# Kernel tuning notes

Measured on AMD Instinct MI355X. Metric: run time of the kernel, lower is better.

The kernel has to match this reference:

```python
import jax, jax.numpy as jnp
import numpy as np

H = 16  # hidden size = time_slot(=32) / 2
G = 3 * H  # gate dim (r|z|n), torch gate order


def _gru_dir(x, Wi, Wh, bi, bh, reverse):
    """Single-direction GRU over time. x: [B,T,F]; Wi:[3H,F]; Wh:[3H,H]."""
    xp = jnp.einsum('btf,gf->btg', x, Wi) + bi  # [B,T,3H] input projections, all steps at once
    if reverse:
        xp = xp[:, ::-1]
    xp_t = jnp.swapaxes(xp, 0, 1)  # [T,B,3H]
    h0 = jnp.zeros((x.shape[0], H), x.dtype)

    def step(h, g_x):
        g_h = h @ Wh.T + bh  # [B,3H]
        r = jax.nn.sigmoid(g_x[:, :H] + g_h[:, :H])
        z = jax.nn.sigmoid(g_x[:, H:2 * H] + g_h[:, H:2 * H])
        n = jnp.tanh(g_x[:, 2 * H:] + r * g_h[:, 2 * H:])
        h_new = (1.0 - z) * n + z * h
        return h_new, h_new

    _, ys = jax.lax.scan(step, h0, xp_t)
    ys = jnp.swapaxes(ys, 0, 1)  # [B,T,H]
    if reverse:
        ys = ys[:, ::-1]
    return ys


def _bigru(x, Wi, Wh, bi, bh):
    """Bidirectional GRU layer; params indexed [dir(2), ...]."""
    fwd = _gru_dir(x, Wi[0], Wh[0], bi[0], bh[0], False)
    bwd = _gru_dir(x, Wi[1], Wh[1], bi[1], bh[1], True)
    return jnp.concatenate([fwd, bwd], axis=-1)  # [B,T,2H]


def setup_inputs() -> dict:
    key = jax.random.key(0)
    ks = jax.random.split(key, 12)
    B, T, F_IN, DEPTH, NCLS = 16384, 64, 3, 5, 4
    s = 0.25  # ~1/sqrt(H) torch init scale
    return {
        'x': jax.random.normal(ks[0], (B, T, F_IN), jnp.float32),
        # GRU1: 1 layer, 2 directions, input 3
        'Wi1': jax.random.normal(ks[1], (2, G, F_IN), jnp.float32) * s,
        'Wh1': jax.random.normal(ks[2], (2, G, H), jnp.float32) * s,
        'bi1': jax.random.normal(ks[3], (2, G), jnp.float32) * s,
        'bh1': jax.random.normal(ks[4], (2, G), jnp.float32) * s,
        # GRU5: 5 layers, 2 directions, input 2H=32 every layer
        'Wi5': jax.random.normal(ks[5], (DEPTH, 2, G, 2 * H), jnp.float32) * s,
        'Wh5': jax.random.normal(ks[6], (DEPTH, 2, G, H), jnp.float32) * s,
        'bi5': jax.random.normal(ks[7], (DEPTH, 2, G), jnp.float32) * s,
        'bh5': jax.random.normal(ks[8], (DEPTH, 2, G), jnp.float32) * s,
        # classifier Linear(2H -> num_class)
        'Wc': jax.random.normal(ks[9], (NCLS, 2 * H), jnp.float32) * s,
        'bc': jax.random.normal(ks[10], (NCLS,), jnp.float32) * s,
    }


def reference(x, Wi1, Wh1, bi1, bh1, Wi5, Wh5, bi5, bh5, Wc, bc):
    y = _bigru(x, Wi1, Wh1, bi1, bh1)  # [B,T,2H]
    for l in range(Wi5.shape[0]):  # 5 stacked bi-GRU layers
        y = _bigru(y, Wi5[l], Wh5[l], bi5[l], bh5[l])
    logits = jnp.einsum('btd,cd->btc', y, Wc) + bc  # [B,T,num_class]
    return jax.nn.softmax(logits, axis=2)
```

## Files before the change

kernel.cpp:

```cpp
#include <hip/hip_runtime.h>

#define T 64
#define F_IN 3
#define H 16
#define G 48
#define D2 32
#define DEPTH 5
#define NCLS 4
#define L2E 1.44269504f

#define YST 32
#define YSB 2048
#define HZ_ZOFF 64

typedef _Float16 half8 __attribute__((ext_vector_type(8)));
typedef float f32x4v __attribute__((ext_vector_type(4)));

__device__ __forceinline__ float fexp2(float x) { return __builtin_amdgcn_exp2f(x); }
__device__ __forceinline__ float frcp(float x)  { return __builtin_amdgcn_rcpf(x); }

__global__ __launch_bounds__(128, 3) void bigru_all(
    const float* __restrict__ x,
    const float* __restrict__ Wi1, const float* __restrict__ Wh1,
    const float* __restrict__ bi1, const float* __restrict__ bh1,
    const float* __restrict__ Wi5, const float* __restrict__ Wh5,
    const float* __restrict__ bi5, const float* __restrict__ bh5,
    const float* __restrict__ Wc,  const float* __restrict__ bc,
    float* __restrict__ out)
{
    __shared__ __align__(16) _Float16 yb[2][2 * YSB];
    __shared__ __align__(16) _Float16 hzb[2][80];
    __shared__ __align__(16) float xls[2][512];

    const int wv   = threadIdx.x >> 6;
    const int lane = threadIdx.x & 63;
    const int pair = blockIdx.x * 2 + wv;

    _Float16* ybw  = yb[wv];
    _Float16* hzbw = hzb[wv];
    float*    xlsw = xls[wv];

    const int j15  = lane & 15;
    const int quad = lane >> 4;
    const int lb   = quad & 1;
    const int dir  = quad >> 1;
    const bool isf = (dir == 0);

    hzbw[lane] = (_Float16)0.0f;
    if (lane < 16) hzbw[64 + lane] = (_Float16)0.0f;

    {
        const float* xg0 = x + (size_t)pair * (2 * T * F_IN);
        #pragma unroll
        for (int k = 0; k < 2; ++k) {
            int idx = lane + 64 * k;
            float a0 = xg0[3 * idx], a1 = xg0[3 * idx + 1], a2 = xg0[3 * idx + 2];
            float4 v; v.x = a0; v.y = a1; v.z = a2; v.w = 0.0f;
            *(float4*)(xlsw + 4 * idx) = v;
        }
    }

    const int  job_a  = j15 >> 2;
    const bool avalid = ((j15 >> 3) == 0) ? (quad < 2) : (quad >= 2);
    const _Float16* aptr = hzbw + (avalid ? (job_a * 16 + (quad & 1) * 8) : HZ_ZOFF);

    const int ystep = isf ? YST : -YST;
    const f32x4v zC = {0.f, 0.f, 0.f, 0.f};
    const int klo = (quad & 1) * 8;
    const int bdir = (quad < 2) ? 0 : 1;

    float hj;
    half8 ag = *(const half8*)aptr;

    {
        half8 whB[3];
        {
            const float* wsrc = Wh1 + bdir * (G * H);
            #pragma unroll
            for (int g = 0; g < 3; ++g) {
                const float scale = (g == 2) ? (-2.0f * L2E) : L2E;
                const float* w = wsrc + (g * 16 + j15) * H + klo;
                half8 hv;
                #pragma unroll
                for (int i = 0; i < 8; ++i) hv[i] = (_Float16)(scale * w[i]);
                whB[g] = hv;
            }
        }
        float wi[3][F_IN];
        float bir[3], bhn2;
        {
            const float* Wi = Wi1 + dir * (G * F_IN);
            const float* bi = bi1 + dir * G;
            const float* bh = bh1 + dir * G;
            #pragma unroll
            for (int g = 0; g < 3; ++g) {
                const float scale = (g == 2) ? (-2.0f * L2E) : L2E;
                int row = g * H + j15;
                #pragma unroll
                for (int k = 0; k < F_IN; ++k) wi[g][k] = scale * Wi[row * F_IN + k];
                bir[g] = scale * bi[row] + ((g < 2) ? (L2E * bh[row]) : 0.0f);
            }
            bhn2 = -2.0f * L2E * bh[2 * H + j15];
        }
        const f32x4v cN = {bhn2, bhn2, bhn2, bhn2};
        hj = 0.0f;

        int xi = lb * 64 + (isf ? 0 : (T - 1));
        const int xstep = isf ? 1 : -1;
        _Float16* yw = ybw + lb * YSB + (isf ? 0 : (T - 1)) * YST + dir * H + j15;

        #pragma unroll 4
        for (int s = 0; s < T; ++s) {
            float4 xv = *(const float4*)(xlsw + 4 * xi);
            xi += xstep;
            float gxr = fmaf(wi[0][2], xv.z, fmaf(wi[0][1], xv.y, fmaf(wi[0][0], xv.x, bir[0])));
            float gxz = fmaf(wi[1][2], xv.z, fmaf(wi[1][1], xv.y, fmaf(wi[1][0], xv.x, bir[1])));
            float gxn = fmaf(wi[2][2], xv.z, fmaf(wi[2][1], xv.y, fmaf(wi[2][0], xv.x, bir[2])));
            f32x4v d0 = __builtin_amdgcn_mfma_f32_16x16x32_f16(ag, whB[0], zC, 0, 0, 0);
            f32x4v d1 = __builtin_amdgcn_mfma_f32_16x16x32_f16(ag, whB[1], zC, 0, 0, 0);
            f32x4v d2 = __builtin_amdgcn_mfma_f32_16x16x32_f16(ag, whB[2], cN, 0, 0, 0);
            float av = gxr + d0[0];
            float bv = gxz + d1[0];
            float Er = fexp2(-av);
            float Ez = fexp2(-bv);
            float rg = frcp(1.0f + Er);
            float c2 = fmaf(rg, d2[0], gxn);
            float Ec = fexp2(c2);
            float dz = 1.0f + Ez;
            float num = fmaf(hj - Ez, Ec, hj + Ez);
            float den = fmaf(dz, Ec, dz);
            float hn = num * frcp(den);
            hj = hn;
            _Float16 hh = (_Float16)hn;
            hzbw[lane] = hh;
            ag = *(const half8*)aptr;
            *yw = hh;
            yw += ystep;
        }
    }

    #pragma unroll 1
    for (int l = 0; l < DEPTH; ++l) {
        half8 bflo[3], bfhi[3];
        #pragma unroll
        for (int g = 0; g < 3; ++g) {
            const float scale = (g == 2) ? (-2.0f * L2E) : L2E;
            const float* w = Wi5 + ((size_t)(l * 2 + bdir) * G + g * 16 + j15) * D2;
            half8 lo, hi;
            #pragma unroll
            for (int i = 0; i < 8; ++i) {
                lo[i] = (_Float16)(scale * w[klo + i]);
                hi[i] = (_Float16)(scale * w[16 + klo + i]);
            }
            bflo[g] = lo;
            bfhi[g] = hi;
        }
        half8 whB[3];
        {
            const float* wsrc = Wh5 + ((size_t)(l * 2) + bdir) * G * H;
            #pragma unroll
            for (int g = 0; g < 3; ++g) {
                const float scale = (g == 2) ? (-2.0f * L2E) : L2E;
                const float* w = wsrc + (g * 16 + j15) * H + klo;
                half8 hv;
                #pragma unroll
                for (int i = 0; i < 8; ++i) hv[i] = (_Float16)(scale * w[i]);
                whB[g] = hv;
            }
        }
        float bib0, bib1, bib2, bhn2;
        {
            const float* biL = bi5 + (l * 2 + dir) * G;
            const float* bhL = bh5 + (l * 2 + dir) * G;
            bib0 = L2E * (biL[j15]     + bhL[j15]);
            bib1 = L2E * (biL[H + j15] + bhL[H + j15]);
            bib2 = -2.0f * L2E * biL[2 * H + j15];
            bhn2 = -2.0f * L2E * bhL[2 * H + j15];
        }
        const f32x4v cR  = {bib0, bib0, bib0, bib0};
        const f32x4v cZ  = {bib1, bib1, bib1, bib1};
        const f32x4v cNx = {bib2, bib2, bib2, bib2};
        const f32x4v cN  = {bhn2, bhn2, bhn2, bhn2};

        hj = 0.0f;
        hzbw[lane] = (_Float16)0.0f;
        ag = *(const half8*)aptr;

        const bool fsel = (j15 < 8);
        const int  lb_a = (j15 >> 2) & 1;
        const int  tl_a = j15 & 3;
        const bool axv  = fsel ? (quad < 2) : (quad >= 2);

        const _Float16* ap;
        int apstep, hioff;
        if (axv) {
            ap     = ybw + lb_a * YSB + (fsel ? tl_a : (T - 1 - tl_a)) * YST + klo;
            apstep = fsel ? (4 * YST) : -(4 * YST);
            hioff  = 16;
        } else {
            ap     = hzbw + HZ_ZOFF;
            apstep = 0;
            hioff  = 0;
        }

        unsigned int ypk[16];

        #pragma unroll
        for (int c = 0; c < 8; ++c) {
            half8 alo = *(const half8*)ap;
            half8 ahi = *(const half8*)(ap + hioff);
            ap += apstep;
            f32x4v c0 = __builtin_amdgcn_mfma_f32_16x16x32_f16(alo, bflo[0], cR, 0, 0, 0);
            f32x4v c1 = __builtin_amdgcn_mfma_f32_16x16x32_f16(alo, bflo[1], cZ, 0, 0, 0);
            f32x4v c2g = __builtin_amdgcn_mfma_f32_16x16x32_f16(alo, bflo[2], cNx, 0, 0, 0);
            c0  = __builtin_amdgcn_mfma_f32_16x16x32_f16(ahi, bfhi[0], c0, 0, 0, 0);
            c1  = __builtin_amdgcn_mfma_f32_16x16x32_f16(ahi, bfhi[1], c1, 0, 0, 0);
            c2g = __builtin_amdgcn_mfma_f32_16x16x32_f16(ahi, bfhi[2], c2g, 0, 0, 0);

            #pragma unroll
            for (int s = 0; s < 4; ++s) {
                f32x4v d0 = __builtin_amdgcn_mfma_f32_16x16x32_f16(ag, whB[0], c0, 0, 0, 0);
                f32x4v d1 = __builtin_amdgcn_mfma_f32_16x16x32_f16(ag, whB[1], c1, 0, 0, 0);
                f32x4v d2 = __builtin_amdgcn_mfma_f32_16x16x32_f16(ag, whB[2], cN, 0, 0, 0);
                float Er = fexp2(-d0[s]);
                float Ez = fexp2(-d1[s]);
                float rg = frcp(1.0f + Er);
                float cc = fmaf(rg, d2[0], c2g[s]);
                float Ec = fexp2(cc);
                float dz = 1.0f + Ez;
                float num = fmaf(hj - Ez, Ec, hj + Ez);
                float den = fmaf(dz, Ec, dz);
                float hn = num * frcp(den);
                hj = hn;
                _Float16 hh = (_Float16)hn;
                hzbw[lane] = hh;
                ag = *(const half8*)aptr;
                unsigned int hb16 = (unsigned int)__builtin_bit_cast(unsigned short, hh);
                if (s & 1) ypk[2 * c + (s >> 1)] |= hb16 << 16;
                else       ypk[2 * c + (s >> 1)]  = hb16;
            }
        }

        {
            _Float16* yw = ybw + lb * YSB + (isf ? 32 : 31) * YST + dir * H + j15;
            #pragma unroll 1
            for (int c = 8; c < 16; ++c) {
                half8 alo = *(const half8*)ap;
                half8 ahi = *(const half8*)(ap + hioff);
                ap += apstep;
                f32x4v c0 = __builtin_amdgcn_mfma_f32_16x16x32_f16(alo, bflo[0], cR, 0, 0, 0);
                f32x4v c1 = __builtin_amdgcn_mfma_f32_16x16x32_f16(alo, bflo[1], cZ, 0, 0, 0);
                f32x4v c2g = __builtin_amdgcn_mfma_f32_16x16x32_f16(alo, bflo[2], cNx, 0, 0, 0);
                c0  = __builtin_amdgcn_mfma_f32_16x16x32_f16(ahi, bfhi[0], c0, 0, 0, 0);
                c1  = __builtin_amdgcn_mfma_f32_16x16x32_f16(ahi, bfhi[1], c1, 0, 0, 0);
                c2g = __builtin_amdgcn_mfma_f32_16x16x32_f16(ahi, bfhi[2], c2g, 0, 0, 0);

                unsigned int w01 = 0, w23 = 0;
                #pragma unroll
                for (int s = 0; s < 4; ++s) {
                    f32x4v d0 = __builtin_amdgcn_mfma_f32_16x16x32_f16(ag, whB[0], c0, 0, 0, 0);
                    f32x4v d1 = __builtin_amdgcn_mfma_f32_16x16x32_f16(ag, whB[1], c1, 0, 0, 0);
                    f32x4v d2 = __builtin_amdgcn_mfma_f32_16x16x32_f16(ag, whB[2], cN, 0, 0, 0);
                    float Er = fexp2(-d0[s]);
                    float Ez = fexp2(-d1[s]);
                    float rg = frcp(1.0f + Er);
                    float cc = fmaf(rg, d2[0], c2g[s]);
                    float Ec = fexp2(cc);
                    float dz = 1.0f + Ez;
                    float num = fmaf(hj - Ez, Ec, hj + Ez);
                    float den = fmaf(dz, Ec, dz);
                    float hn = num * frcp(den);
                    hj = hn;
                    _Float16 hh = (_Float16)hn;
                    hzbw[lane] = hh;
                    ag = *(const half8*)aptr;
                    unsigned int hb16 = (unsigned int)__builtin_bit_cast(unsigned short, hh);
                    if (s & 1) { if (s >> 1) w23 |= hb16 << 16; else w01 |= hb16 << 16; }
                    else       { if (s >> 1) w23  = hb16;       else w01  = hb16; }
                }
                *yw = __builtin_bit_cast(_Float16, (unsigned short)(w01 & 0xffffu)); yw += ystep;
                *yw = __builtin_bit_cast(_Float16, (unsigned short)(w01 >> 16));     yw += ystep;
                *yw = __builtin_bit_cast(_Float16, (unsigned short)(w23 & 0xffffu)); yw += ystep;
                *yw = __builtin_bit_cast(_Float16, (unsigned short)(w23 >> 16));     yw += ystep;
            }
        }

        {
            _Float16* yw = ybw + lb * YSB + (isf ? 0 : (T - 1)) * YST + dir * H + j15;
            #pragma unroll
            for (int i = 0; i < 16; ++i) {
                unsigned int v = ypk[i];
                *yw = __builtin_bit_cast(_Float16, (unsigned short)(v & 0xffffu));
                yw += ystep;
                *yw = __builtin_bit_cast(_Float16, (unsigned short)(v >> 16));
                yw += ystep;
            }
        }
    }

    #pragma unroll
    for (int i = 0; i < 2; ++i) {
        int idx = lane + i * 64;
        int bb  = idx >> 6;
        int t   = idx & 63;
        const _Float16* yrow = ybw + bb * YSB + t * YST;
        float yv[D2];
        #pragma unroll
        for (int k8 = 0; k8 < 4; ++k8) {
            half8 v = *(const half8*)(yrow + k8 * 8);
            #pragma unroll
            for (int i8 = 0; i8 < 8; ++i8) yv[k8 * 8 + i8] = (float)v[i8];
        }
        float lg[NCLS];
        #pragma unroll
        for (int c = 0; c < NCLS; ++c) {
            const float* wc = Wc + c * D2;
            float acc = bc[c];
            #pragma unroll
            for (int k = 0; k < D2; ++k) acc = fmaf(wc[k], yv[k], acc);
            lg[c] = acc;
        }
        float m = fmaxf(fmaxf(lg[0], lg[1]), fmaxf(lg[2], lg[3]));
        float e0 = __expf(lg[0] - m), e1 = __expf(lg[1] - m);
        float e2 = __expf(lg[2] - m), e3 = __expf(lg[3] - m);
        float inv = frcp(e0 + e1 + e2 + e3);
        size_t bglob = (size_t)pair * 2 + bb;
        float4 o;
        o.x = e0 * inv; o.y = e1 * inv; o.z = e2 * inv; o.w = e3 * inv;
        ((float4*)out)[bglob * T + t] = o;
    }
}

extern "C" void kernel_launch(void* const* d_in, const int* in_sizes, int n_in,
                              void* d_out, int out_size, void* d_ws, size_t ws_size,
                              hipStream_t stream) {
    const float* x   = (const float*)d_in[0];
    const float* Wi1 = (const float*)d_in[1];
    const float* Wh1 = (const float*)d_in[2];
    const float* bi1 = (const float*)d_in[3];
    const float* bh1 = (const float*)d_in[4];
    const float* Wi5 = (const float*)d_in[5];
    const float* Wh5 = (const float*)d_in[6];
    const float* bi5 = (const float*)d_in[7];
    const float* bh5 = (const float*)d_in[8];
    const float* Wc  = (const float*)d_in[9];
    const float* bc  = (const float*)d_in[10];
    float* out = (float*)d_out;

    const int B = in_sizes[0] / (T * F_IN);
    dim3 grid(B / 4), block(128);
    hipLaunchKernelGGL(bigru_all, grid, block, 0, stream,
                       x, Wi1, Wh1, bi1, bh1, Wi5, Wh5, bi5, bh5, Wc, bc, out);
}
```

Baseline: 310.3 us.

## Ping-pong LDS sequence buffers and launch one wave per block

Each block now runs a single wavefront on one batch pair. A double-buffered LDS area (P0/P1) alternates source and destination per layer, so each layer writes its hidden states straight to the other buffer. This replaces the old scheme that parked the first half of the outputs in registers (ypk) and split the time loop into two variants. The goal is lower register pressure, simpler code and removal of the inter-wave shared-memory layout. The cost is more LDS per wavefront (about 16 KB versus about 10 KB before), which may limit how many waves fit on a CU.

```diff
diff --git a/kernel.cpp b/kernel.cpp
--- a/kernel.cpp
+++ b/kernel.cpp
@@ -19,7 +19,7 @@
 __device__ __forceinline__ float fexp2(float x) { return __builtin_amdgcn_exp2f(x); }
 __device__ __forceinline__ float frcp(float x)  { return __builtin_amdgcn_rcpf(x); }
 
-__global__ __launch_bounds__(128, 3) void bigru_all(
+__global__ __launch_bounds__(64, 3) void bigru_all(
     const float* __restrict__ x,
     const float* __restrict__ Wi1, const float* __restrict__ Wh1,
     const float* __restrict__ bi1, const float* __restrict__ bh1,
@@ -28,18 +28,13 @@
     const float* __restrict__ Wc,  const float* __restrict__ bc,
     float* __restrict__ out)
 {
-    __shared__ __align__(16) _Float16 yb[2][2 * YSB];
-    __shared__ __align__(16) _Float16 hzb[2][80];
-    __shared__ __align__(16) float xls[2][512];
-
-    const int wv   = threadIdx.x >> 6;
-    const int lane = threadIdx.x & 63;
-    const int pair = blockIdx.x * 2 + wv;
-
-    _Float16* ybw  = yb[wv];
-    _Float16* hzbw = hzb[wv];
-    float*    xlsw = xls[wv];
-
+    __shared__ __align__(16) _Float16 S[4 * YSB + 80];
+    _Float16* const P0   = S;
+    _Float16* const P1   = S + 2 * YSB;
+    _Float16* const hzbw = S + 4 * YSB;
+    float*    const xlsw = (float*)P1;
+
+    const int lane = threadIdx.x;
     const int j15  = lane & 15;
     const int quad = lane >> 4;
     const int lb   = quad & 1;
@@ -50,7 +45,7 @@
     if (lane < 16) hzbw[64 + lane] = (_Float16)0.0f;
 
     {
-        const float* xg0 = x + (size_t)pair * (2 * T * F_IN);
+        const float* xg0 = x + (size_t)blockIdx.x * (2 * T * F_IN);
         #pragma unroll
         for (int k = 0; k < 2; ++k) {
             int idx = lane + 64 * k;
@@ -107,7 +102,7 @@
 
         int xi = lb * 64 + (isf ? 0 : (T - 1));
         const int xstep = isf ? 1 : -1;
-        _Float16* yw = ybw + lb * YSB + (isf ? 0 : (T - 1)) * YST + dir * H + j15;
+        _Float16* yw = P0 + lb * YSB + (isf ? 0 : (T - 1)) * YST + dir * H + j15;
 
         #pragma unroll 4
         for (int s = 0; s < T; ++s) {
@@ -141,6 +136,9 @@
 
     #pragma unroll 1
     for (int l = 0; l < DEPTH; ++l) {
+        _Float16* const ysrc = (l & 1) ? P1 : P0;
+        _Float16* const ydst = (l & 1) ? P0 : P1;
+
         half8 bflo[3], bfhi[3];
         #pragma unroll
         for (int g = 0; g < 3; ++g) {
@@ -194,7 +192,7 @@
         const _Float16* ap;
         int apstep, hioff;
         if (axv) {
-            ap     = ybw + lb_a * YSB + (fsel ? tl_a : (T - 1 - tl_a)) * YST + klo;
+            ap     = ysrc + lb_a * YSB + (fsel ? tl_a : (T - 1 - tl_a)) * YST + klo;
             apstep = fsel ? (4 * YST) : -(4 * YST);
             hioff  = 16;
         } else {
@@ -203,10 +201,9 @@
             hioff  = 0;
         }
 
-        unsigned int ypk[16];
-
-        #pragma unroll
-        for (int c = 0; c < 8; ++c) {
+        _Float16* yw = ydst + lb * YSB + (isf ? 0 : (T - 1)) * YST + dir * H + j15;
+        #pragma unroll 4
+        for (int c = 0; c < 16; ++c) {
             half8 alo = *(const half8*)ap;
             half8 ahi = *(const half8*)(ap + hioff);
             ap += apstep;
@@ -235,64 +232,7 @@
                 _Float16 hh = (_Float16)hn;
                 hzbw[lane] = hh;
                 ag = *(const half8*)aptr;
-                unsigned int hb16 = (unsigned int)__builtin_bit_cast(unsigned short, hh);
-                if (s & 1) ypk[2 * c + (s >> 1)] |= hb16 << 16;
-                else       ypk[2 * c + (s >> 1)]  = hb16;
-            }
-        }
-
-        {
-            _Float16* yw = ybw + lb * YSB + (isf ? 32 : 31) * YST + dir * H + j15;
-            #pragma unroll 1
-            for (int c = 8; c < 16; ++c) {
-                half8 alo = *(const half8*)ap;
-                half8 ahi = *(const half8*)(ap + hioff);
-                ap += apstep;
-                f32x4v c0 = __builtin_amdgcn_mfma_f32_16x16x32_f16(alo, bflo[0], cR, 0, 0, 0);
-                f32x4v c1 = __builtin_amdgcn_mfma_f32_16x16x32_f16(alo, bflo[1], cZ, 0, 0, 0);
-                f32x4v c2g = __builtin_amdgcn_mfma_f32_16x16x32_f16(alo, bflo[2], cNx, 0, 0, 0);
-                c0  = __builtin_amdgcn_mfma_f32_16x16x32_f16(ahi, bfhi[0], c0, 0, 0, 0);
-                c1  = __builtin_amdgcn_mfma_f32_16x16x32_f16(ahi, bfhi[1], c1, 0, 0, 0);
-                c2g = __builtin_amdgcn_mfma_f32_16x16x32_f16(ahi, bfhi[2], c2g, 0, 0, 0);
-
-                unsigned int w01 = 0, w23 = 0;
-                #pragma unroll
-                for (int s = 0; s < 4; ++s) {
-                    f32x4v d0 = __builtin_amdgcn_mfma_f32_16x16x32_f16(ag, whB[0], c0, 0, 0, 0);
-                    f32x4v d1 = __builtin_amdgcn_mfma_f32_16x16x32_f16(ag, whB[1], c1, 0, 0, 0);
-                    f32x4v d2 = __builtin_amdgcn_mfma_f32_16x16x32_f16(ag, whB[2], cN, 0, 0, 0);
-                    float Er = fexp2(-d0[s]);
-                    float Ez = fexp2(-d1[s]);
-                    float rg = frcp(1.0f + Er);
-                    float cc = fmaf(rg, d2[0], c2g[s]);
-                    float Ec = fexp2(cc);
-                    float dz = 1.0f + Ez;
-                    float num = fmaf(hj - Ez, Ec, hj + Ez);
-                    float den = fmaf(dz, Ec, dz);
-                    float hn = num * frcp(den);
-                    hj = hn;
-                    _Float16 hh = (_Float16)hn;
-                    hzbw[lane] = hh;
-                    ag = *(const half8*)aptr;
-                    unsigned int hb16 = (unsigned int)__builtin_bit_cast(unsigned short, hh);
-                    if (s & 1) { if (s >> 1) w23 |= hb16 << 16; else w01 |= hb16 << 16; }
-                    else       { if (s >> 1) w23  = hb16;       else w01  = hb16; }
-                }
-                *yw = __builtin_bit_cast(_Float16, (unsigned short)(w01 & 0xffffu)); yw += ystep;
-                *yw = __builtin_bit_cast(_Float16, (unsigned short)(w01 >> 16));     yw += ystep;
-                *yw = __builtin_bit_cast(_Float16, (unsigned short)(w23 & 0xffffu)); yw += ystep;
-                *yw = __builtin_bit_cast(_Float16, (unsigned short)(w23 >> 16));     yw += ystep;
-            }
-        }
-
-        {
-            _Float16* yw = ybw + lb * YSB + (isf ? 0 : (T - 1)) * YST + dir * H + j15;
-            #pragma unroll
-            for (int i = 0; i < 16; ++i) {
-                unsigned int v = ypk[i];
-                *yw = __builtin_bit_cast(_Float16, (unsigned short)(v & 0xffffu));
-                yw += ystep;
-                *yw = __builtin_bit_cast(_Float16, (unsigned short)(v >> 16));
+                *yw = hh;
                 yw += ystep;
             }
         }
@@ -303,7 +243,7 @@
         int idx = lane + i * 64;
         int bb  = idx >> 6;
         int t   = idx & 63;
-        const _Float16* yrow = ybw + bb * YSB + t * YST;
+        const _Float16* yrow = P1 + bb * YSB + t * YST;
         float yv[D2];
         #pragma unroll
         for (int k8 = 0; k8 < 4; ++k8) {
@@ -324,7 +264,7 @@
         float e0 = __expf(lg[0] - m), e1 = __expf(lg[1] - m);
         float e2 = __expf(lg[2] - m), e3 = __expf(lg[3] - m);
         float inv = frcp(e0 + e1 + e2 + e3);
-        size_t bglob = (size_t)pair * 2 + bb;
+        size_t bglob = (size_t)blockIdx.x * 2 + bb;
         float4 o;
         o.x = e0 * inv; o.y = e1 * inv; o.z = e2 * inv; o.w = e3 * inv;
         ((float4*)out)[bglob * T + t] = o;
@@ -348,7 +288,7 @@
     float* out = (float*)d_out;
 
     const int B = in_sizes[0] / (T * F_IN);
-    dim3 grid(B / 4), block(128);
+    dim3 grid(B / 2), block(64);
     hipLaunchKernelGGL(bigru_all, grid, block, 0, stream,
                        x, Wi1, Wh1, bi1, bh1, Wi5, Wh5, bi5, bh5, Wc, bc, out);
 }
```

Measured after the change: 353.9 us. 1.14x slower.
